# Kernel tuning notes

Hardware: AMD Instinct MI355X
Metric: run time of the kernel (lower is better)

The kernel has to match this reference:

```python
import jax, jax.numpy as jnp
import numpy as np

B, T = 32, 8192
RNN, ENC, ATT, LOC, K = 1024, 512, 128, 32, 31


def setup_inputs() -> dict:
    key = jax.random.key(0)
    ks = jax.random.split(key, 9)
    return {
        'queries': jax.random.normal(ks[0], (B, RNN), jnp.float32),
        'memories': jax.random.normal(ks[1], (B, ENC, T), jnp.float32),
        'processed_memories': jax.random.normal(ks[2], (B, ATT, T), jnp.float32),
        'previous_alignments': jax.random.uniform(ks[3], (B, T), jnp.float32),
        'cumulated_alignments': jax.random.uniform(ks[4], (B, T), jnp.float32),
        'masks': jnp.zeros((B, T), jnp.bool_),
        # learned params (xavier-ish scale)
        'w_query': jax.random.normal(ks[5], (ATT, RNN), jnp.float32) * (1.0 / np.sqrt(RNN)),
        'w_loc_conv': jax.random.normal(ks[6], (LOC, 2, K), jnp.float32) * (1.0 / np.sqrt(2 * K)),
        'w_loc_1x1': jax.random.normal(ks[7], (ATT, LOC), jnp.float32) * (1.0 / np.sqrt(LOC)),
        'w_score': jax.random.normal(ks[8], (ATT,), jnp.float32) * (1.0 / np.sqrt(ATT)),
    }


def reference(queries, memories, processed_memories, previous_alignments,
              cumulated_alignments, masks, w_query, w_loc_conv, w_loc_1x1, w_score):
    # ---- Calc_Score ----
    # Query 1x1 conv == matmul: [B, ATT, 1]
    q = (queries @ w_query.T)[:, :, None]
    # Location features: conv over [B, 2, T] (same padding), then 1x1 -> [B, ATT, T]
    attn_cat = jnp.stack([previous_alignments, cumulated_alignments], axis=1)  # [B,2,T]
    pad = (K - 1) // 2
    loc = jax.lax.conv_general_dilated(attn_cat, w_loc_conv, (1,), [(pad, pad)],
                                       dimension_numbers=('NCH', 'OIH', 'NCH'))  # [B,LOC,T]
    loc = jnp.einsum('blt,al->bat', loc, w_loc_1x1)  # [B,ATT,T]
    scores = jnp.einsum('bat,a->bt', jnp.tanh(q + processed_memories + loc), w_score)  # [B,T]
    # ---- Apply_Score (sigmoid_noise = 0) ----
    scores = jnp.where(masks, -jnp.finfo(scores.dtype).max, scores)
    p = jax.nn.sigmoid(scores)  # p_choose_i, [B,T]
    # stepwise monotonic update: a_t = prev*p + shift_right(prev*(1-p))
    shifted = jnp.pad((previous_alignments * (1.0 - p))[:, :-1], ((0, 0), (1, 0)))
    alignments = previous_alignments * p + shifted  # [B,T]
    contexts = jnp.einsum('bt,bct->bc', alignments, memories)  # [B,ENC]
    return contexts, alignments
```

## Files before the change

kernel.cpp:

```cpp
#include <hip/hip_runtime.h>
#include <math.h>

#define B_   32
#define T_   8192
#define RNN_ 1024
#define ENC_ 512
#define ATT_ 128
#define LOC_ 32
#define K_   31
#define PAD_ 15

typedef __fp16 half2v __attribute__((ext_vector_type(2)));

__device__ __forceinline__ float fdot2(unsigned int a, unsigned int b, float c) {
    return __builtin_amdgcn_fdot2(__builtin_bit_cast(half2v, a),
                                  __builtin_bit_cast(half2v, b), c, false);
}

__device__ __forceinline__ unsigned int packh2(float x, float y) {
    half2v h;
    h.x = (__fp16)x;
    h.y = (__fp16)y;
    return __builtin_bit_cast(unsigned int, h);
}

__device__ __forceinline__ float fast_tanh(float x) {
    x = fminf(15.f, fmaxf(-15.f, x));
    float e = __expf(2.f * x);
    return (e - 1.f) * __builtin_amdgcn_rcpf(e + 1.f);
}

__device__ __forceinline__ float fast_sigmoid(float x) {
    x = fminf(30.f, fmaxf(-30.f, x));
    float e = __expf(-x);
    return __builtin_amdgcn_rcpf(1.f + e);
}

__global__ __launch_bounds__(256) void k_prep_query(const float* __restrict__ queries,
                                                    const float* __restrict__ wq,
                                                    const float* __restrict__ wconv,
                                                    const float* __restrict__ w1,
                                                    float* __restrict__ qout,
                                                    unsigned int* __restrict__ wTh2,
                                                    unsigned int* __restrict__ w1h2) {
    if (blockIdx.x == (B_ * ATT_) / 4) {
        for (int i = threadIdx.x; i < K_ * LOC_; i += blockDim.x) {
            int k = i / LOC_;
            int l = i % LOC_;
            float wp = wconv[l * (2 * K_) + k];
            float wc = wconv[l * (2 * K_) + K_ + k];
            wTh2[i] = packh2(wp, wc);
        }
        for (int i = threadIdx.x; i < ATT_ * (LOC_ / 2); i += blockDim.x) {
            int a = i / (LOC_ / 2);
            int p = i % (LOC_ / 2);
            w1h2[i] = packh2(w1[a * LOC_ + 2 * p], w1[a * LOC_ + 2 * p + 1]);
        }
        return;
    }
    int w    = blockIdx.x * 4 + (threadIdx.x >> 6);
    int lane = threadIdx.x & 63;
    int b = w >> 7, a = w & 127;
    const float4* qrow = (const float4*)(queries + (size_t)b * RNN_);
    const float4* wrow = (const float4*)(wq + (size_t)a * RNN_);
    float acc = 0.f;
#pragma unroll
    for (int i = 0; i < 4; ++i) {
        float4 x = qrow[i * 64 + lane];
        float4 y = wrow[i * 64 + lane];
        acc += x.x * y.x + x.y * y.y + x.z * y.z + x.w * y.w;
    }
#pragma unroll
    for (int off = 32; off; off >>= 1) acc += __shfl_xor(acc, off);
    if (lane == 0) qout[b * ATT_ + a] = acc;
}

#define BLK2  256
#define TILE2 256

__global__ __launch_bounds__(256) void k_score(
    const float* __restrict__ pm,
    const float* __restrict__ prev,
    const float* __restrict__ cum,
    const unsigned char* __restrict__ masks,
    const float* __restrict__ qbuf,
    const unsigned int* __restrict__ wTh2,
    const unsigned int* __restrict__ w1h2,
    const float* __restrict__ wsc,
    float* __restrict__ pout)
{
    __shared__ unsigned int sPC[TILE2 + K_ - 1];
    int blk  = blockIdx.x;
    int b    = blk >> 5;
    int tile = blk & 31;
    int tbase = tile * TILE2;
    const float* prow = prev + (size_t)b * T_;
    const float* crow = cum + (size_t)b * T_;
    for (int i = threadIdx.x; i < TILE2 + K_ - 1; i += BLK2) {
        int g = tbase - PAD_ + i;
        bool ok = (g >= 0) && (g < T_);
        float pv = ok ? prow[g] : 0.f;
        float cv = ok ? crow[g] : 0.f;
        sPC[i] = packh2(pv, cv);
    }
    __syncthreads();

    int lt = threadIdx.x;
    int t0 = tbase + lt;

    float loc[LOC_];
#pragma unroll
    for (int l = 0; l < LOC_; ++l) loc[l] = 0.f;

    for (int k = 0; k < K_; ++k) {
        unsigned int pc = sPC[lt + k];
        const uint4* wk4 = (const uint4*)(wTh2 + k * LOC_);
#pragma unroll
        for (int lq = 0; lq < 8; ++lq) {
            uint4 wv = wk4[lq];
            loc[4 * lq + 0] = fdot2(wv.x, pc, loc[4 * lq + 0]);
            loc[4 * lq + 1] = fdot2(wv.y, pc, loc[4 * lq + 1]);
            loc[4 * lq + 2] = fdot2(wv.z, pc, loc[4 * lq + 2]);
            loc[4 * lq + 3] = fdot2(wv.w, pc, loc[4 * lq + 3]);
        }
    }

    unsigned int lh[LOC_ / 2];
#pragma unroll
    for (int i = 0; i < LOC_ / 2; ++i)
        lh[i] = packh2(loc[2 * i], loc[2 * i + 1]);

    float sc0 = 0.f, sc1 = 0.f, sc2 = 0.f, sc3 = 0.f;
    const float* pmb = pm + (size_t)b * ATT_ * T_ + t0;
    const float* qb  = qbuf + b * ATT_;
#pragma unroll 4
    for (int a = 0; a < ATT_; ++a) {
        float q   = qb[a];
        float wsa = wsc[a];
        const uint4* wa4 = (const uint4*)(w1h2 + a * (LOC_ / 2));
        float pmv = pmb[(size_t)a * T_];
        float l2a = 0.f, l2b = 0.f;
        uint4 w0 = wa4[0];
        uint4 w1v = wa4[1];
        uint4 w2 = wa4[2];
        uint4 w3 = wa4[3];
        l2a = fdot2(w0.x, lh[0],  l2a);  l2b = fdot2(w1v.x, lh[4],  l2b);
        l2a = fdot2(w0.y, lh[1],  l2a);  l2b = fdot2(w1v.y, lh[5],  l2b);
        l2a = fdot2(w0.z, lh[2],  l2a);  l2b = fdot2(w1v.z, lh[6],  l2b);
        l2a = fdot2(w0.w, lh[3],  l2a);  l2b = fdot2(w1v.w, lh[7],  l2b);
        l2a = fdot2(w2.x, lh[8],  l2a);  l2b = fdot2(w3.x, lh[12], l2b);
        l2a = fdot2(w2.y, lh[9],  l2a);  l2b = fdot2(w3.y, lh[13], l2b);
        l2a = fdot2(w2.z, lh[10], l2a);  l2b = fdot2(w3.z, lh[14], l2b);
        l2a = fdot2(w2.w, lh[11], l2a);  l2b = fdot2(w3.w, lh[15], l2b);
        float term = wsa * fast_tanh(q + pmv + l2a + l2b);
        switch (a & 3) {
            case 0: sc0 += term; break;
            case 1: sc1 += term; break;
            case 2: sc2 += term; break;
            default: sc3 += term; break;
        }
    }
    float score = (sc0 + sc1) + (sc2 + sc3);

    unsigned char m = masks[(size_t)b * T_ + t0];
    float s = m ? -3.0e38f : score;
    pout[(size_t)b * T_ + t0] = fast_sigmoid(s);
}

__global__ __launch_bounds__(256) void k_align(const float* __restrict__ p,
                                               const float* __restrict__ prev,
                                               float* __restrict__ align) {
    int idx = blockIdx.x * blockDim.x + threadIdx.x;
    int b  = idx / (T_ / 4);
    int t0 = (idx % (T_ / 4)) * 4;
    const float* pr = p + (size_t)b * T_;
    const float* vr = prev + (size_t)b * T_;
    float4 p4 = *(const float4*)(pr + t0);
    float4 v4 = *(const float4*)(vr + t0);
    float pm1 = (t0 > 0) ? pr[t0 - 1] : 0.f;
    float vm1 = (t0 > 0) ? vr[t0 - 1] : 0.f;
    float4 o;
    o.x = v4.x * p4.x + vm1 * (1.f - pm1);
    o.y = v4.y * p4.y + v4.x * (1.f - p4.x);
    o.z = v4.z * p4.z + v4.y * (1.f - p4.y);
    o.w = v4.w * p4.w + v4.z * (1.f - p4.z);
    *(float4*)(align + (size_t)b * T_ + t0) = o;
}

__global__ __launch_bounds__(256) void k_context(const float* __restrict__ mem,
                                                 const float* __restrict__ align,
                                                 float* __restrict__ ctx) {
    int w    = blockIdx.x * 4 + (threadIdx.x >> 6);
    int lane = threadIdx.x & 63;
    int b = w >> 9;
    int c = w & 511;
    const float4* mrow = (const float4*)(mem + ((size_t)b * ENC_ + c) * T_);
    const float4* arow = (const float4*)(align + (size_t)b * T_);
    float acc0 = 0.f, acc1 = 0.f;
#pragma unroll 8
    for (int i = 0; i < T_ / 256; ++i) {
        float4 m = mrow[i * 64 + lane];
        float4 a = arow[i * 64 + lane];
        if (i & 1)
            acc1 += m.x * a.x + m.y * a.y + m.z * a.z + m.w * a.w;
        else
            acc0 += m.x * a.x + m.y * a.y + m.z * a.z + m.w * a.w;
    }
    float acc = acc0 + acc1;
#pragma unroll
    for (int off = 32; off; off >>= 1) acc += __shfl_xor(acc, off);
    if (lane == 0) ctx[b * ENC_ + c] = acc;
}

extern "C" void kernel_launch(void* const* d_in, const int* in_sizes, int n_in,
                              void* d_out, int out_size, void* d_ws, size_t ws_size,
                              hipStream_t stream) {
    const float* queries = (const float*)d_in[0];
    const float* memories = (const float*)d_in[1];
    const float* pm = (const float*)d_in[2];
    const float* prev = (const float*)d_in[3];
    const float* cum = (const float*)d_in[4];
    const unsigned char* masks = (const unsigned char*)d_in[5];
    const float* w_query = (const float*)d_in[6];
    const float* w_conv = (const float*)d_in[7];
    const float* w_1x1 = (const float*)d_in[8];
    const float* w_score = (const float*)d_in[9];

    float* out_ctx = (float*)d_out;
    float* out_align = (float*)d_out + (size_t)B_ * ENC_;

    float* ws_q = (float*)d_ws;
    float* ws_p = ws_q + B_ * ATT_;
    unsigned int* ws_wTh2 = (unsigned int*)(ws_p + (size_t)B_ * T_);
    unsigned int* ws_w1h2 = ws_wTh2 + K_ * LOC_ + 32;

    hipLaunchKernelGGL(k_prep_query, dim3((B_ * ATT_) / 4 + 1), dim3(256), 0, stream,
                       queries, w_query, w_conv, w_1x1, ws_q, ws_wTh2, ws_w1h2);
    hipLaunchKernelGGL(k_score, dim3(B_ * (T_ / TILE2)), dim3(BLK2), 0, stream,
                       pm, prev, cum, masks, ws_q, ws_wTh2, ws_w1h2, w_score, ws_p);
    hipLaunchKernelGGL(k_align, dim3((B_ * T_ / 4) / 256), dim3(256), 0, stream,
                       ws_p, prev, out_align);
    hipLaunchKernelGGL(k_context, dim3((B_ * ENC_) / 4), dim3(256), 0, stream,
                       memories, out_align, out_ctx);
}
```

Baseline: 162.8 us.

## Double-buffer processed_memories tiles into LDS via async global_load_lds

```diff
diff --git a/kernel.cpp b/kernel.cpp
--- a/kernel.cpp
+++ b/kernel.cpp
@@ -34,6 +34,12 @@
     x = fminf(30.f, fmaxf(-30.f, x));
     float e = __expf(-x);
     return __builtin_amdgcn_rcpf(1.f + e);
+}
+
+__device__ __forceinline__ void gload_lds16(const float* g, float* l) {
+    __builtin_amdgcn_global_load_lds(
+        (const __attribute__((address_space(1))) void*)g,
+        (__attribute__((address_space(3))) void*)l, 16, 0, 0);
 }
 
 __global__ __launch_bounds__(256) void k_prep_query(const float* __restrict__ queries,
@@ -77,6 +83,8 @@
 
 #define BLK2  256
 #define TILE2 256
+#define ACH   16
+#define NCH   (ATT_ / ACH)
 
 __global__ __launch_bounds__(256) void k_score(
     const float* __restrict__ pm,
@@ -89,79 +97,103 @@
     const float* __restrict__ wsc,
     float* __restrict__ pout)
 {
+    __shared__ float sPM[2][ACH][TILE2];
     __shared__ unsigned int sPC[TILE2 + K_ - 1];
+
     int blk  = blockIdx.x;
     int b    = blk >> 5;
     int tile = blk & 31;
     int tbase = tile * TILE2;
+    int tid  = threadIdx.x;
+    int lane = tid & 63;
+    int wv   = tid >> 6;
+
     const float* prow = prev + (size_t)b * T_;
     const float* crow = cum + (size_t)b * T_;
-    for (int i = threadIdx.x; i < TILE2 + K_ - 1; i += BLK2) {
+    for (int i = tid; i < TILE2 + K_ - 1; i += BLK2) {
         int g = tbase - PAD_ + i;
         bool ok = (g >= 0) && (g < T_);
-        float pv = ok ? prow[g] : 0.f;
-        float cv = ok ? crow[g] : 0.f;
-        sPC[i] = packh2(pv, cv);
+        sPC[i] = packh2(ok ? prow[g] : 0.f, ok ? crow[g] : 0.f);
+    }
+
+    const float* pmt = pm + (size_t)b * ATT_ * T_ + tbase;
+#pragma unroll
+    for (int r = 0; r < 4; ++r) {
+        int a = wv * 4 + r;
+        gload_lds16(pmt + (size_t)a * T_ + 4 * lane, &sPM[0][a][0]);
     }
     __syncthreads();
 
-    int lt = threadIdx.x;
+    int lt = tid;
     int t0 = tbase + lt;
 
     float loc[LOC_];
-#pragma unroll
-    for (int l = 0; l < LOC_; ++l) loc[l] = 0.f;
-
-    for (int k = 0; k < K_; ++k) {
-        unsigned int pc = sPC[lt + k];
-        const uint4* wk4 = (const uint4*)(wTh2 + k * LOC_);
-#pragma unroll
-        for (int lq = 0; lq < 8; ++lq) {
-            uint4 wv = wk4[lq];
-            loc[4 * lq + 0] = fdot2(wv.x, pc, loc[4 * lq + 0]);
-            loc[4 * lq + 1] = fdot2(wv.y, pc, loc[4 * lq + 1]);
-            loc[4 * lq + 2] = fdot2(wv.z, pc, loc[4 * lq + 2]);
-            loc[4 * lq + 3] = fdot2(wv.w, pc, loc[4 * lq + 3]);
-        }
-    }
-
     unsigned int lh[LOC_ / 2];
-#pragma unroll
-    for (int i = 0; i < LOC_ / 2; ++i)
-        lh[i] = packh2(loc[2 * i], loc[2 * i + 1]);
-
     float sc0 = 0.f, sc1 = 0.f, sc2 = 0.f, sc3 = 0.f;
-    const float* pmb = pm + (size_t)b * ATT_ * T_ + t0;
-    const float* qb  = qbuf + b * ATT_;
+    const float* qb = qbuf + b * ATT_;
+
+    for (int c = 0; c < NCH; ++c) {
+        if (c + 1 < NCH) {
+#pragma unroll
+            for (int r = 0; r < 4; ++r) {
+                int a = (c + 1) * ACH + wv * 4 + r;
+                gload_lds16(pmt + (size_t)a * T_ + 4 * lane,
+                            &sPM[(c + 1) & 1][wv * 4 + r][0]);
+            }
+        }
+        if (c == 0) {
+#pragma unroll
+            for (int l = 0; l < LOC_; ++l) loc[l] = 0.f;
+            for (int k = 0; k < K_; ++k) {
+                unsigned int pc = sPC[lt + k];
+                const uint4* wk4 = (const uint4*)(wTh2 + k * LOC_);
+#pragma unroll
+                for (int lq = 0; lq < 8; ++lq) {
+                    uint4 wv4 = wk4[lq];
+                    loc[4 * lq + 0] = fdot2(wv4.x, pc, loc[4 * lq + 0]);
+                    loc[4 * lq + 1] = fdot2(wv4.y, pc, loc[4 * lq + 1]);
+                    loc[4 * lq + 2] = fdot2(wv4.z, pc, loc[4 * lq + 2]);
+                    loc[4 * lq + 3] = fdot2(wv4.w, pc, loc[4 * lq + 3]);
+                }
+            }
+#pragma unroll
+            for (int i = 0; i < LOC_ / 2; ++i)
+                lh[i] = packh2(loc[2 * i], loc[2 * i + 1]);
+        }
+
+        const float* spm = &sPM[c & 1][0][0];
 #pragma unroll 4
-    for (int a = 0; a < ATT_; ++a) {
-        float q   = qb[a];
-        float wsa = wsc[a];
-        const uint4* wa4 = (const uint4*)(w1h2 + a * (LOC_ / 2));
-        float pmv = pmb[(size_t)a * T_];
-        float l2a = 0.f, l2b = 0.f;
-        uint4 w0 = wa4[0];
-        uint4 w1v = wa4[1];
-        uint4 w2 = wa4[2];
-        uint4 w3 = wa4[3];
-        l2a = fdot2(w0.x, lh[0],  l2a);  l2b = fdot2(w1v.x, lh[4],  l2b);
-        l2a = fdot2(w0.y, lh[1],  l2a);  l2b = fdot2(w1v.y, lh[5],  l2b);
-        l2a = fdot2(w0.z, lh[2],  l2a);  l2b = fdot2(w1v.z, lh[6],  l2b);
-        l2a = fdot2(w0.w, lh[3],  l2a);  l2b = fdot2(w1v.w, lh[7],  l2b);
-        l2a = fdot2(w2.x, lh[8],  l2a);  l2b = fdot2(w3.x, lh[12], l2b);
-        l2a = fdot2(w2.y, lh[9],  l2a);  l2b = fdot2(w3.y, lh[13], l2b);
-        l2a = fdot2(w2.z, lh[10], l2a);  l2b = fdot2(w3.z, lh[14], l2b);
-        l2a = fdot2(w2.w, lh[11], l2a);  l2b = fdot2(w3.w, lh[15], l2b);
-        float term = wsa * fast_tanh(q + pmv + l2a + l2b);
-        switch (a & 3) {
-            case 0: sc0 += term; break;
-            case 1: sc1 += term; break;
-            case 2: sc2 += term; break;
-            default: sc3 += term; break;
-        }
-    }
+        for (int aa = 0; aa < ACH; ++aa) {
+            int a = c * ACH + aa;
+            float q   = qb[a];
+            float wsa = wsc[a];
+            const uint4* wa4 = (const uint4*)(w1h2 + a * (LOC_ / 2));
+            float pmv = spm[aa * TILE2 + lt];
+            float l2a = 0.f, l2b = 0.f;
+            uint4 w0 = wa4[0];
+            uint4 w1v = wa4[1];
+            uint4 w2 = wa4[2];
+            uint4 w3 = wa4[3];
+            l2a = fdot2(w0.x, lh[0],  l2a);  l2b = fdot2(w1v.x, lh[4],  l2b);
+            l2a = fdot2(w0.y, lh[1],  l2a);  l2b = fdot2(w1v.y, lh[5],  l2b);
+            l2a = fdot2(w0.z, lh[2],  l2a);  l2b = fdot2(w1v.z, lh[6],  l2b);
+            l2a = fdot2(w0.w, lh[3],  l2a);  l2b = fdot2(w1v.w, lh[7],  l2b);
+            l2a = fdot2(w2.x, lh[8],  l2a);  l2b = fdot2(w3.x, lh[12], l2b);
+            l2a = fdot2(w2.y, lh[9],  l2a);  l2b = fdot2(w3.y, lh[13], l2b);
+            l2a = fdot2(w2.z, lh[10], l2a);  l2b = fdot2(w3.z, lh[14], l2b);
+            l2a = fdot2(w2.w, lh[11], l2a);  l2b = fdot2(w3.w, lh[15], l2b);
+            float term = wsa * fast_tanh(q + pmv + l2a + l2b);
+            switch (aa & 3) {
+                case 0: sc0 += term; break;
+                case 1: sc1 += term; break;
+                case 2: sc2 += term; break;
+                default: sc3 += term; break;
+            }
+        }
+        __syncthreads();
+    }
+
     float score = (sc0 + sc1) + (sc2 + sc3);
-
     unsigned char m = masks[(size_t)b * T_ + t0];
     float s = m ? -3.0e38f : score;
     pout[(size_t)b * T_ + t0] = fast_sigmoid(s);
```

Result: slower. 167.0 us (+2.6%).
